# Optimization experiments

Measured on AMD Instinct MI355X. Metric: run time of the kernel, lower is better.

## Reference

```python
import jax, jax.numpy as jnp
import numpy as np

B, S, DIM, H, HD, R = 4, 1024, 2048, 32, 64, 16
START = S  # start_pos == segment_size: memory-update + full-segment branch


def elu1(x):
    # F.elu(x) + 1, positive feature map for compressive memory
    return jnp.where(x > 0, x + 1.0, jnp.exp(jnp.minimum(x, 0.0)))


def rope(t, cos, sin):
    # t: [B, S, H, D]; cos/sin: [S, D/2]; matches torch view_as_complex pairing
    tr = t.reshape(t.shape[:-1] + (-1, 2))
    a, b = tr[..., 0], tr[..., 1]
    c = cos[None, :, None, :]
    s = sin[None, :, None, :]
    out = jnp.stack([a * c - b * s, a * s + b * c], axis=-1)
    return out.reshape(t.shape)


def setup_inputs() -> dict:
    key = jax.random.key(0)
    ks = jax.random.split(key, 24)
    nrm = lambda k, shp, sc=1.0: jax.random.normal(k, shp, dtype=jnp.float32) * sc
    x = nrm(ks[0], (B, S, DIM))
    prompt_query = nrm(ks[1], (B, 1, H, HD))
    cache_k = nrm(ks[2], (B, S, H, HD))
    cache_v = nrm(ks[3], (B, S, H, HD))
    memory_long = nrm(ks[4], (B, H, HD, HD), 0.1)
    memory_query = nrm(ks[5], (B, H, HD, HD), 0.1)
    norm_term = jax.random.uniform(ks[6], (B, H, HD), dtype=jnp.float32) * float(S) + 1.0
    pos = jnp.arange(S, dtype=jnp.float32) + float(START)
    inv = 1.0 / (10000.0 ** (jnp.arange(0, HD, 2, dtype=jnp.float32) / HD))
    ang = pos[:, None] * inv[None, :]
    freqs_cos = jnp.cos(ang).astype(jnp.float32)
    freqs_sin = jnp.sin(ang).astype(jnp.float32)
    causal = jnp.tril(jnp.ones((S, S), dtype=bool))
    mask = jnp.where(causal, 0.0, -1e9).astype(jnp.float32)[None, None]
    sc = 1.0 / np.sqrt(DIM)
    wq = nrm(ks[7], (DIM, DIM), sc)
    wk = nrm(ks[8], (DIM, DIM), sc)
    wv = nrm(ks[9], (DIM, DIM), sc)
    wo = nrm(ks[10], (DIM, DIM), sc)
    lq1 = nrm(ks[11], (R, DIM), sc); lq2 = nrm(ks[12], (DIM, R), 0.01)
    lk1 = nrm(ks[13], (R, DIM), sc); lk2 = nrm(ks[14], (DIM, R), 0.01)
    lv1 = nrm(ks[15], (R, DIM), sc); lv2 = nrm(ks[16], (DIM, R), 0.01)
    lo1 = nrm(ks[17], (R, DIM), sc); lo2 = nrm(ks[18], (DIM, R), 0.01)
    gate = jnp.zeros((1, H, 1, 1), dtype=jnp.float32)
    gmem_w = nrm(ks[19], (1, HD), 0.1)
    gmem_b = jnp.zeros((1,), dtype=jnp.float32)
    return dict(x=x, prompt_query=prompt_query, cache_k=cache_k, cache_v=cache_v,
                memory_long=memory_long, memory_query=memory_query, norm_term=norm_term,
                freqs_cos=freqs_cos, freqs_sin=freqs_sin, mask=mask,
                wq=wq, wk=wk, wv=wv, wo=wo,
                lq1=lq1, lq2=lq2, lk1=lk1, lk2=lk2, lv1=lv1, lv2=lv2, lo1=lo1, lo2=lo2,
                gate=gate, gmem_w=gmem_w, gmem_b=gmem_b, start_pos=START)


def reference(x, prompt_query, cache_k, cache_v, memory_long, memory_query, norm_term,
              freqs_cos, freqs_sin, mask, wq, wk, wv, wo,
              lq1, lq2, lk1, lk2, lv1, lv2, lo1, lo2, gate, gmem_w, gmem_b, start_pos):
    b, s, dim = x.shape
    h = gate.shape[1]
    hd = dim // h
    # LoRA-augmented QKV projections
    xq = x @ wq.T + (x @ lq1.T) @ lq2.T
    xk = x @ wk.T + (x @ lk1.T) @ lk2.T
    xv = x @ wv.T + (x @ lv1.T) @ lv2.T
    xq = xq.reshape(b, s, h, hd)
    xk = xk.reshape(b, s, h, hd)
    xv = xv.reshape(b, s, h, hd)
    q = xq.transpose(0, 2, 1, 3)  # [B,H,S,D]
    # --- memory update from previous segment cache (start_pos >= segment_size) ---
    up_k = cache_k.transpose(0, 2, 1, 3)  # [B,H,S,D]
    up_v = cache_v.transpose(0, 2, 1, 3)
    pq = prompt_query.transpose(0, 2, 1, 3)[:, :, 0, :]  # [B,H,D]
    q_scores = jnp.einsum('bhd,bhsd->bhs', pq, up_k) / np.sqrt(hd)
    query_f_v = up_v * jax.nn.sigmoid(q_scores)[..., None]  # gated value stream
    sigma_k = elu1(up_k)
    mem_l = memory_long + jnp.einsum('bhsd,bhse->bhde', sigma_k, up_v)
    mem_q = memory_query + jnp.einsum('bhsd,bhse->bhde', sigma_k, query_f_v)
    nrm_t = norm_term + sigma_k.sum(axis=2)  # [B,H,D]
    # --- retrieve from compressive memory with pre-RoPE queries ---
    sigma_q = elu1(q)
    denom = jnp.einsum('bhsd,bhd->bhs', sigma_q, nrm_t)[..., None]
    mem_out = jnp.einsum('bhsd,bhde->bhse', sigma_q, mem_l) / denom
    qmem_out = jnp.einsum('bhsd,bhde->bhse', sigma_q, mem_q) / denom
    # --- local causal attention on current segment ---
    qr = rope(xq, freqs_cos, freqs_sin).transpose(0, 2, 1, 3)
    kr = rope(xk, freqs_cos, freqs_sin).transpose(0, 2, 1, 3)
    v = xv.transpose(0, 2, 1, 3)
    scores = jnp.einsum('bhqd,bhkd->bhqk', qr, kr) / np.sqrt(hd) + mask
    probs = jax.nn.softmax(scores, axis=-1)
    attn = jnp.einsum('bhqk,bhkd->bhqd', probs, v)
    # --- gated combination of memory and local attention ---
    g_q = jax.nn.sigmoid(jnp.einsum('bhsd,od->bhso', qmem_out, gmem_w) + gmem_b)
    mem_comb = mem_out + g_q * qmem_out
    g = jax.nn.sigmoid(gate)
    out = g * mem_comb + (1.0 - g) * attn
    out = out.transpose(0, 2, 1, 3).reshape(b, s, dim)
    return out @ wo.T + (out @ lo1.T) @ lo2.T
```

## Files before the change

kernel.cpp:

```cpp
#include <hip/hip_runtime.h>
#include <hip/hip_bf16.h>

typedef __hip_bfloat16 bf16;
typedef __attribute__((ext_vector_type(8))) short short8;
typedef __attribute__((ext_vector_type(4))) float floatx4;

#define B_ 4
#define S_ 1024
#define DIM_ 2048
#define H_ 32
#define HD_ 64
#define R_ 16
#define BS_ (B_*S_)

typedef __attribute__((address_space(1))) void GVoid;
typedef __attribute__((address_space(3))) void LVoid;
#define GLDS16(gp, lp) __builtin_amdgcn_global_load_lds((GVoid*)(gp), (LVoid*)(lp), 16, 0, 0)

__device__ __forceinline__ float b2f(bf16 v){ return __bfloat162float(v); }
__device__ __forceinline__ float elu1f(float x){ return x > 0.f ? x + 1.f : __expf(x); }
__device__ __forceinline__ float sigmoidf(float x){ return 1.f/(1.f + __expf(-x)); }
__device__ __forceinline__ float loadf(bf16 v){ return __bfloat162float(v); }
__device__ __forceinline__ float loadf(float v){ return v; }

__device__ __forceinline__ float dread(const void* p, size_t i, int f){
    float r;
    if (f) r = __bfloat162float(((const bf16*)p)[i]);
    else   r = ((const float*)p)[i];
    return r;
}
__device__ __forceinline__ void dwrite(void* p, size_t i, float v, int f){
    if (f) ((bf16*)p)[i] = __float2bfloat16(v);
    else   ((float*)p)[i] = v;
}

__global__ void detect_kernel(const void* __restrict__ x, int* __restrict__ flag){
    __shared__ int cnt[256];
    int t = threadIdx.x;
    int c = 0;
    for (int i = t; i < 4096; i += 256){
        float v = __bfloat162float(((const bf16*)x)[i]);
        float a = fabsf(v);
        if (a > 1e-3f && a < 1e3f) c++;
    }
    cnt[t] = c;
    __syncthreads();
    if (t == 0){
        int s = 0;
        for (int i = 0; i < 256; ++i) s += cnt[i];
        *flag = (s > 3686) ? 1 : 0;
    }
}

__global__ void convert_kernel(const void* __restrict__ src, bf16* __restrict__ dst,
                               int n, const int* __restrict__ flagp){
    int i = (blockIdx.x * 256 + threadIdx.x) * 8;
    if (i >= n) return;
    short8 o;
    if (*flagp){
        o = *(const short8*)((const bf16*)src + i);
    } else {
        const float* s = (const float*)src + i;
        #pragma unroll
        for (int j = 0; j < 8; ++j)
            ((bf16*)&o)[j] = __float2bfloat16(s[j]);
    }
    *(short8*)(dst + i) = o;
}

template<typename T>
__device__ __forceinline__ void wprep_body(const T* __restrict__ W,
                                           const T* __restrict__ L1,
                                           const T* __restrict__ L2,
                                           bf16* __restrict__ dst){
    int n = blockIdx.y;
    int k = blockIdx.x * 256 + threadIdx.x;
    size_t nk = (size_t)n * DIM_ + k;
    float acc = loadf(W[nk]);
    #pragma unroll
    for (int r = 0; r < 16; ++r)
        acc += loadf(L2[n*16 + r]) * loadf(L1[(size_t)r*DIM_ + k]);
    dst[nk] = __float2bfloat16(acc);
}
__global__ __launch_bounds__(256)
void wprep_kernel(const void* __restrict__ W, const void* __restrict__ L1,
                  const void* __restrict__ L2, const int* __restrict__ flagp,
                  bf16* __restrict__ dst){
    if (*flagp) wprep_body((const bf16*)W, (const bf16*)L1, (const bf16*)L2, dst);
    else        wprep_body((const float*)W, (const float*)L1, (const float*)L2, dst);
}

template<int CMODE>
__global__ __launch_bounds__(256)
void gemm_mfma_kernel(const bf16* __restrict__ A, const bf16* __restrict__ Bw,
                      const int* __restrict__ flagp, void* __restrict__ C) {
    __shared__ bf16 Als[128*32];
    __shared__ bf16 Bls[128*32];
    int tid = threadIdx.x;
    int w = tid >> 6, lane = tid & 63;
    int wr = w >> 1, wc = w & 1;
    int rm0 = blockIdx.y * 128;
    int cn0 = blockIdx.x * 128;

    const bf16* gA = A  + (size_t)(rm0 + w*32 + (lane>>2)) * DIM_ + (lane&3)*8;
    const bf16* gB = Bw + (size_t)(cn0 + w*32 + (lane>>2)) * DIM_ + (lane&3)*8;
    bf16* lA0 = Als + (w*32)*32;
    bf16* lA1 = Als + (w*32+16)*32;
    bf16* lB0 = Bls + (w*32)*32;
    bf16* lB1 = Bls + (w*32+16)*32;

    floatx4 acc[4][4];
    #pragma unroll
    for (int i = 0; i < 4; ++i)
        #pragma unroll
        for (int j = 0; j < 4; ++j) acc[i][j] = (floatx4){0.f,0.f,0.f,0.f};

    int aoff[4], boff[4];
    #pragma unroll
    for (int i = 0; i < 4; ++i) {
        aoff[i] = (wr*64 + i*16 + (lane&15))*32 + (lane>>4)*8;
        boff[i] = (wc*64 + i*16 + (lane&15))*32 + (lane>>4)*8;
    }

    for (int kk = 0; kk < DIM_; kk += 32) {
        GLDS16(gA + kk,             lA0);
        GLDS16(gA + 16*DIM_ + kk,   lA1);
        GLDS16(gB + kk,             lB0);
        GLDS16(gB + 16*DIM_ + kk,   lB1);
        __syncthreads();
        short8 af[4], bf_[4];
        #pragma unroll
        for (int i = 0; i < 4; ++i) {
            af[i]  = *(const short8*)(Als + aoff[i]);
            bf_[i] = *(const short8*)(Bls + boff[i]);
        }
        #pragma unroll
        for (int i = 0; i < 4; ++i)
            #pragma unroll
            for (int j = 0; j < 4; ++j)
                acc[i][j] = __builtin_amdgcn_mfma_f32_16x16x32_bf16(
                    af[i], bf_[j], acc[i][j], 0, 0, 0);
        __syncthreads();
    }

    int f = (CMODE==0) ? *flagp : 1;
    #pragma unroll
    for (int i = 0; i < 4; ++i) {
        #pragma unroll
        for (int reg = 0; reg < 4; ++reg) {
            int m_loc = wr*64 + i*16 + (lane>>4)*4 + reg;
            #pragma unroll
            for (int j = 0; j < 4; ++j) {
                int n_loc = wc*64 + j*16 + (lane&15);
                float val = acc[i][j][reg];
                size_t idx = (size_t)(rm0 + m_loc) * DIM_ + cn0 + n_loc;
                if (CMODE==1) ((bf16*)C)[idx] = __float2bfloat16(val);
                else          dwrite(C, idx, val, f);
            }
        }
    }
}

__global__ void qscore_kernel(const void* __restrict__ pq, const void* __restrict__ ck,
                              const int* __restrict__ flagp, float* __restrict__ qsig) {
    int f = *flagp;
    int tid = threadIdx.x;
    int lane = tid & 63;
    int wid = (blockIdx.x << 2) | (tid >> 6);
    int s = wid & (S_-1);
    int h = (wid >> 10) & (H_-1);
    int b = wid >> 15;
    float p = dread(pq, ((size_t)b*H_ + h)*HD_ + lane, f);
    float k = dread(ck, (((size_t)b*S_ + s)*H_ + h)*HD_ + lane, f);
    float v = p * k;
    for (int off = 32; off; off >>= 1) v += __shfl_xor(v, off, 64);
    if (lane == 0) qsig[((size_t)b*H_ + h)*S_ + s] = sigmoidf(v * 0.125f);
}

__global__ __launch_bounds__(256)
void mem_kernel(const void* __restrict__ ck, const void* __restrict__ cv,
                const float* __restrict__ qsig,
                const int* __restrict__ flagp,
                float* __restrict__ pbufL, float* __restrict__ pbufQ,
                float* __restrict__ pbufN) {
    int f = *flagp;
    __shared__ float ks[4][64], vs[4][64], fv[4][64];
    int bh = blockIdx.x;
    int st = blockIdx.y;
    int b = bh >> 5, h = bh & 31;
    int t = threadIdx.x;
    int e = t & 63;
    int dg = t >> 6;
    float accL[16] = {};
    float accQ[16] = {};
    float nsum = 0.f;
    int sbase = st * 128;
    for (int s0 = 0; s0 < 128; s0 += 4) {
        int sl = t >> 6, d = t & 63;
        int s = sbase + s0 + sl;
        size_t base = (((size_t)b*S_ + s)*H_ + h)*HD_ + d;
        float kv = elu1f(dread(ck, base, f));
        float vv = dread(cv, base, f);
        float sg = qsig[((size_t)b*H_ + h)*S_ + s];
        ks[sl][d] = kv;
        vs[sl][d] = vv;
        fv[sl][d] = vv * sg;
        __syncthreads();
        #pragma unroll
        for (int s2 = 0; s2 < 4; ++s2) {
            float ve = vs[s2][e];
            float fe = fv[s2][e];
            #pragma unroll
            for (int dd = 0; dd < 16; ++dd) {
                float kk = ks[s2][dg*16 + dd];
                accL[dd] += kk * ve;
                accQ[dd] += kk * fe;
            }
        }
        if (t < 64) {
            #pragma unroll
            for (int s2 = 0; s2 < 4; ++s2) nsum += ks[s2][t];
        }
        __syncthreads();
    }
    size_t pb = ((size_t)bh*8 + st) * 4096;
    #pragma unroll
    for (int dd = 0; dd < 16; ++dd) {
        int d = dg*16 + dd;
        pbufL[pb + d*64 + e] = accL[dd];
        pbufQ[pb + d*64 + e] = accQ[dd];
    }
    if (t < 64) pbufN[((size_t)bh*8 + st)*64 + t] = nsum;
}

__global__ __launch_bounds__(256)
void memreduce_kernel(const float* __restrict__ pbufL, const float* __restrict__ pbufQ,
                      const float* __restrict__ pbufN,
                      const void* __restrict__ meml_in, const void* __restrict__ memq_in,
                      const void* __restrict__ norm_in, const int* __restrict__ flagp,
                      float* __restrict__ meml, float* __restrict__ memq,
                      float* __restrict__ nrmt) {
    int f = *flagp;
    size_t gi = (size_t)blockIdx.x * 256 + threadIdx.x;
    int bh = (int)(gi >> 12);
    int i  = (int)(gi & 4095);
    float sL = dread(meml_in, gi, f);
    float sQ = dread(memq_in, gi, f);
    #pragma unroll
    for (int p = 0; p < 8; ++p) {
        sL += pbufL[((size_t)bh*8 + p)*4096 + i];
        sQ += pbufQ[((size_t)bh*8 + p)*4096 + i];
    }
    meml[gi] = sL;
    memq[gi] = sQ;
    if (i < 64) {
        float sN = dread(norm_in, (size_t)bh*64 + i, f);
        #pragma unroll
        for (int p = 0; p < 8; ++p) sN += pbufN[((size_t)bh*8 + p)*64 + i];
        nrmt[(size_t)bh*64 + i] = sN;
    }
}

__global__ __launch_bounds__(256)
void memout_kernel(const bf16* __restrict__ xq, const float* __restrict__ meml,
                   const float* __restrict__ memq, const float* __restrict__ nrmt,
                   const void* __restrict__ gw, const void* __restrict__ gb,
                   const int* __restrict__ flagp, bf16* __restrict__ memcomb) {
    int f = *flagp;
    __shared__ float Ml[64][64];
    __shared__ float Mq[64][64];
    __shared__ float nr[64];
    __shared__ float gwv[64];
    __shared__ float sq[4][64];
    int bh = blockIdx.x;
    int st = blockIdx.y;
    int b = bh >> 5, h = bh & 31;
    int t = threadIdx.x;
    int w = t >> 6, lane = t & 63;
    size_t mb = (size_t)bh * 4096;
    const floatx4* mlv = (const floatx4*)(meml + mb);
    const floatx4* mqv = (const floatx4*)(memq + mb);
    floatx4* Mlv = (floatx4*)&Ml[0][0];
    floatx4* Mqv = (floatx4*)&Mq[0][0];
    for (int i = t; i < 1024; i += 256) {
        Mlv[i] = mlv[i];
        Mqv[i] = mqv[i];
    }
    if (t < 64) { nr[t] = nrmt[(size_t)bh*64 + t]; gwv[t] = dread(gw, t, f); }
    float gbv = dread(gb, 0, f);
    __syncthreads();
    for (int i = 0; i < 16; ++i) {
        int s = st*64 + i*4 + w;
        float x = b2f(xq[((size_t)(b*S_ + s))*DIM_ + h*64 + lane]);
        float sqv = elu1f(x);
        sq[w][lane] = sqv;
        float dv = sqv * nr[lane];
        for (int off = 32; off; off >>= 1) dv += __shfl_xor(dv, off, 64);
        float mo = 0.f, qmo = 0.f;
        #pragma unroll
        for (int d = 0; d < 64; ++d) {
            float sqd = sq[w][d];
            mo  += sqd * Ml[d][lane];
            qmo += sqd * Mq[d][lane];
        }
        float inv = 1.f / dv;
        mo *= inv; qmo *= inv;
        float gqv = qmo * gwv[lane];
        for (int off = 32; off; off >>= 1) gqv += __shfl_xor(gqv, off, 64);
        float gq = sigmoidf(gqv + gbv);
        memcomb[(((size_t)bh)*S_ + s)*64 + lane] = __float2bfloat16(mo + gq * qmo);
    }
}

__global__ void rope_kernel(bf16* __restrict__ buf, const void* __restrict__ fcos,
                            const void* __restrict__ fsin,
                            const int* __restrict__ flagp) {
    int f = *flagp;
    int pid = (blockIdx.x * 256 + threadIdx.x) * 4;
    int cp = pid & 1023;
    int m  = pid >> 10;
    int s  = m & (S_-1);
    int p  = cp & 31;
    size_t idx = (size_t)m * DIM_ + cp*2;
    short8 v = *(const short8*)(buf + idx);
    short8 o;
    #pragma unroll
    for (int j = 0; j < 4; ++j) {
        float c  = dread(fcos, s*32 + p + j, f);
        float sn = dread(fsin, s*32 + p + j, f);
        float a = b2f(((bf16*)&v)[2*j]);
        float b = b2f(((bf16*)&v)[2*j+1]);
        ((bf16*)&o)[2*j]   = __float2bfloat16(a*c - b*sn);
        ((bf16*)&o)[2*j+1] = __float2bfloat16(a*sn + b*c);
    }
    *(short8*)(buf + idx) = o;
}

__global__ __launch_bounds__(256)
void vtrans_kernel(const bf16* __restrict__ xv, bf16* __restrict__ vtg) {
    __shared__ bf16 tile[64*72];
    int bh = blockIdx.x;
    int b = bh >> 5;
    int s0 = blockIdx.y * 64;
    int tid = threadIdx.x;
    for (int it = tid; it < 512; it += 256) {
        int row = it >> 3, blk = it & 7;
        short8 val = *(const short8*)(xv + (size_t)(b*S_ + s0 + row)*DIM_
                                      + (bh & 31)*64 + blk*8);
        *(short8*)(tile + row*72 + ((blk ^ (row & 7))*8)) = val;
    }
    __syncthreads();
    for (int it = tid; it < 512; it += 256) {
        int d = it >> 3, sb = (it & 7)*8;
        short8 o;
        #pragma unroll
        for (int i = 0; i < 8; ++i) {
            int s = sb + i;
            o[i] = *(const short*)(tile + s*72 + (((d>>3) ^ (s & 7))*8) + (d & 7));
        }
        *(short8*)(vtg + ((size_t)bh*64 + d)*S_ + s0 + sb) = o;
    }
}

__global__ __launch_bounds__(256)
void attn_mfma_kernel(const bf16* __restrict__ qr, const bf16* __restrict__ kr,
                      const bf16* __restrict__ vtg, const bf16* __restrict__ memcomb,
                      const void* __restrict__ gate, const int* __restrict__ flagp,
                      bf16* __restrict__ outc) {
    __shared__ bf16 Qs[64*72];
    __shared__ bf16 Ks[64*72];
    __shared__ bf16 Vt[64*72];
    __shared__ bf16 Ps[4][16*72];
    int bid = blockIdx.x;
    int qt = bid & 15;
    int h  = (bid >> 4) & 31;
    int b  = bid >> 9;
    int q0 = qt * 64;
    int tid = threadIdx.x;
    int w = tid >> 6, lane = tid & 63;
    int quad = lane >> 4, r16 = lane & 15;

    for (int it = tid; it < 512; it += 256) {
        int row = it >> 3, c8 = (it & 7)*8;
        *(short8*)(Qs + row*72 + c8) =
            *(const short8*)(qr + (size_t)(b*S_ + q0 + row)*DIM_ + h*64 + c8);
    }
    __syncthreads();
    short8 qf[2];
    #pragma unroll
    for (int kb = 0; kb < 2; ++kb)
        qf[kb] = *(const short8*)(Qs + (w*16 + r16)*72 + kb*32 + quad*8);

    float mrow[4] = {-1e30f,-1e30f,-1e30f,-1e30f};
    float lrow[4] = {0.f,0.f,0.f,0.f};
    floatx4 Ox[4];
    #pragma unroll
    for (int db = 0; db < 4; ++db) Ox[db] = (floatx4){0.f,0.f,0.f,0.f};

    int ntiles = qt + 1;
    for (int kt = 0; kt < ntiles; ++kt) {
        int k0 = kt * 64;
        for (int it = tid; it < 512; it += 256) {
            int row = it >> 3, c8 = (it & 7)*8;
            *(short8*)(Ks + row*72 + c8) =
                *(const short8*)(kr + (size_t)(b*S_ + k0 + row)*DIM_ + h*64 + c8);
            *(short8*)(Vt + row*72 + c8) =
                *(const short8*)(vtg + ((size_t)(b*H_ + h)*64 + row)*S_ + k0 + c8);
        }
        __syncthreads();

        floatx4 Sbv[4];
        #pragma unroll
        for (int nb = 0; nb < 4; ++nb) {
            floatx4 a = (floatx4){0.f,0.f,0.f,0.f};
            #pragma unroll
            for (int kb = 0; kb < 2; ++kb) {
                short8 kf = *(const short8*)(Ks + (nb*16 + r16)*72 + kb*32 + quad*8);
                a = __builtin_amdgcn_mfma_f32_16x16x32_bf16(qf[kb], kf, a, 0, 0, 0);
            }
            Sbv[nb] = a;
        }
        float S4[4][4];
        #pragma unroll
        for (int nb = 0; nb < 4; ++nb)
            #pragma unroll
            for (int reg = 0; reg < 4; ++reg) {
                int qg = q0 + w*16 + quad*4 + reg;
                int kg = k0 + nb*16 + r16;
                float s = Sbv[nb][reg] * 0.125f;
                S4[nb][reg] = (kg > qg) ? -1e30f : s;
            }
        float alpha[4], rsum[4];
        #pragma unroll
        for (int reg = 0; reg < 4; ++reg) {
            float mx = fmaxf(fmaxf(S4[0][reg], S4[1][reg]),
                             fmaxf(S4[2][reg], S4[3][reg]));
            mx = fmaxf(mx, __shfl_xor(mx, 1, 64));
            mx = fmaxf(mx, __shfl_xor(mx, 2, 64));
            mx = fmaxf(mx, __shfl_xor(mx, 4, 64));
            mx = fmaxf(mx, __shfl_xor(mx, 8, 64));
            float mn = fmaxf(mrow[reg], mx);
            alpha[reg] = __expf(mrow[reg] - mn);
            mrow[reg] = mn;
            float rs = 0.f;
            #pragma unroll
            for (int nb = 0; nb < 4; ++nb) {
                float p = __expf(S4[nb][reg] - mn);
                S4[nb][reg] = p;
                rs += p;
            }
            rs += __shfl_xor(rs, 1, 64);
            rs += __shfl_xor(rs, 2, 64);
            rs += __shfl_xor(rs, 4, 64);
            rs += __shfl_xor(rs, 8, 64);
            rsum[reg] = rs;
            lrow[reg] = lrow[reg]*alpha[reg] + rs;
        }
        #pragma unroll
        for (int nb = 0; nb < 4; ++nb)
            #pragma unroll
            for (int reg = 0; reg < 4; ++reg)
                Ps[w][(quad*4 + reg)*72 + nb*16 + r16] = __float2bfloat16(S4[nb][reg]);
        short8 pf[2];
        #pragma unroll
        for (int kb = 0; kb < 2; ++kb)
            pf[kb] = *(const short8*)(&Ps[w][0] + r16*72 + kb*32 + quad*8);
        #pragma unroll
        for (int db = 0; db < 4; ++db) {
            #pragma unroll
            for (int reg = 0; reg < 4; ++reg) Ox[db][reg] *= alpha[reg];
            #pragma unroll
            for (int kb = 0; kb < 2; ++kb) {
                short8 vf = *(const short8*)(Vt + (db*16 + r16)*72 + kb*32 + quad*8);
                Ox[db] = __builtin_amdgcn_mfma_f32_16x16x32_bf16(pf[kb], vf, Ox[db], 0, 0, 0);
            }
        }
        __syncthreads();
    }

    int f = *flagp;
    float g = sigmoidf(dread(gate, h, f));
    #pragma unroll
    for (int db = 0; db < 4; ++db)
        #pragma unroll
        for (int reg = 0; reg < 4; ++reg) {
            int qg = q0 + w*16 + quad*4 + reg;
            int d  = db*16 + r16;
            float attn = Ox[db][reg] / lrow[reg];
            float comb = b2f(memcomb[((size_t)(b*H_ + h)*S_ + qg)*64 + d]);
            outc[(size_t)(b*S_ + qg)*DIM_ + h*64 + d] =
                __float2bfloat16(g*comb + (1.f - g)*attn);
        }
}

extern "C" void kernel_launch(void* const* d_in, const int* in_sizes, int n_in,
                              void* d_out, int out_size, void* d_ws, size_t ws_size,
                              hipStream_t stream) {
    const void* x        = d_in[0];
    const void* pq       = d_in[1];
    const void* cache_k  = d_in[2];
    const void* cache_v  = d_in[3];
    const void* mem_long = d_in[4];
    const void* mem_qry  = d_in[5];
    const void* norm_t   = d_in[6];
    const void* fcos     = d_in[7];
    const void* fsin     = d_in[8];
    const void* wq  = d_in[10];
    const void* wk  = d_in[11];
    const void* wv  = d_in[12];
    const void* wo  = d_in[13];
    const void* lq1 = d_in[14];
    const void* lq2 = d_in[15];
    const void* lk1 = d_in[16];
    const void* lk2 = d_in[17];
    const void* lv1 = d_in[18];
    const void* lv2 = d_in[19];
    const void* lo1 = d_in[20];
    const void* lo2 = d_in[21];
    const void* gate = d_in[22];
    const void* gmw  = d_in[23];
    const void* gmb  = d_in[24];

    const size_t NBSD = (size_t)BS_ * DIM_;
    const size_t NW   = (size_t)DIM_ * DIM_;
    int*  flag = (int*)d_ws;
    bf16* xb   = (bf16*)((char*)d_ws + 16);
    bf16* wbuf = xb + NBSD;
    bf16* xq   = wbuf + NW;
    bf16* xk   = xq + NBSD;
    bf16* xv   = xk + NBSD;
    bf16* outc = xv + NBSD;
    bf16* vtg  = outc + NBSD;
    float* qsig = (float*)(vtg + NBSD);
    float* meml = qsig + (size_t)B_*H_*S_;
    float* memq = meml + (size_t)B_*H_*HD_*HD_;
    float* nrmt = memq + (size_t)B_*H_*HD_*HD_;
    bf16* memcomb = (bf16*)d_out;

    float* pbufL = (float*)xb;
    float* pbufQ = (float*)outc;
    float* pbufN = (float*)wbuf;

    dim3 ggrid(DIM_/128, BS_/128);
    dim3 wgrid(DIM_/256, DIM_);

    detect_kernel<<<1, 256, 0, stream>>>(x, flag);
    convert_kernel<<<(int)(NBSD/2048), 256, 0, stream>>>(x, xb, (int)NBSD, flag);
    wprep_kernel<<<wgrid, 256, 0, stream>>>(wq, lq1, lq2, flag, wbuf);
    gemm_mfma_kernel<1><<<ggrid, 256, 0, stream>>>(xb, wbuf, flag, xq);
    wprep_kernel<<<wgrid, 256, 0, stream>>>(wk, lk1, lk2, flag, wbuf);
    gemm_mfma_kernel<1><<<ggrid, 256, 0, stream>>>(xb, wbuf, flag, xk);
    wprep_kernel<<<wgrid, 256, 0, stream>>>(wv, lv1, lv2, flag, wbuf);
    gemm_mfma_kernel<1><<<ggrid, 256, 0, stream>>>(xb, wbuf, flag, xv);
    vtrans_kernel<<<dim3(B_*H_, S_/64), 256, 0, stream>>>(xv, vtg);
    qscore_kernel<<<(B_*H_*S_)/4, 256, 0, stream>>>(pq, cache_k, flag, qsig);
    mem_kernel<<<dim3(B_*H_, 8), 256, 0, stream>>>(cache_k, cache_v, qsig, flag,
                                                   pbufL, pbufQ, pbufN);
    memreduce_kernel<<<(B_*H_*HD_*HD_)/256, 256, 0, stream>>>(
        pbufL, pbufQ, pbufN, mem_long, mem_qry, norm_t, flag, meml, memq, nrmt);
    memout_kernel<<<dim3(B_*H_, S_/64), 256, 0, stream>>>(xq, meml, memq, nrmt,
                                                          gmw, gmb, flag, memcomb);
    rope_kernel<<<(BS_*1024)/(256*4), 256, 0, stream>>>(xq, fcos, fsin, flag);
    rope_kernel<<<(BS_*1024)/(256*4), 256, 0, stream>>>(xk, fcos, fsin, flag);
    attn_mfma_kernel<<<B_*H_*(S_/64), 256, 0, stream>>>(xq, xk, vtg, memcomb,
                                                        gate, flag, outc);
    wprep_kernel<<<wgrid, 256, 0, stream>>>(wo, lo1, lo2, flag, wbuf);
    gemm_mfma_kernel<0><<<ggrid, 256, 0, stream>>>(outc, wbuf, flag, d_out);
}
```

Baseline: 838.8 us.

## Batch QKV weight prep and GEMMs, prefetch K/V tiles in causal attention

Merges the three weight-prep kernels and the three QKV projection GEMMs into single launches, with the K and V prepared weights stored in the vtg scratch region. The attention kernel now prefetches the next K/V tile into registers while the current tile computes, and remaps block indices so heavy and light causal tiles interleave. It also adds setprio around the MFMA loops and an XOR swizzle on the P tile in LDS to reduce bank conflicts. The vtg buffer is reused for weights before vtrans overwrites it, so correctness relies on that launch ordering.

Measured after the change: 773.8 us. 7.7% less time.

```diff
diff --git a/kernel.cpp b/kernel.cpp
--- a/kernel.cpp
+++ b/kernel.cpp
@@ -90,6 +90,25 @@
     else        wprep_body((const float*)W, (const float*)L1, (const float*)L2, dst);
 }
 
+__global__ __launch_bounds__(256)
+void wprep3_kernel(const void* __restrict__ W0, const void* __restrict__ W1,
+                   const void* __restrict__ W2,
+                   const void* __restrict__ L1q, const void* __restrict__ L1k,
+                   const void* __restrict__ L1v,
+                   const void* __restrict__ L2q, const void* __restrict__ L2k,
+                   const void* __restrict__ L2v,
+                   const int* __restrict__ flagp,
+                   bf16* __restrict__ d0, bf16* __restrict__ d1,
+                   bf16* __restrict__ d2){
+    int z = blockIdx.z;
+    const void* W  = (z==0) ? W0 : (z==1) ? W1 : W2;
+    const void* L1 = (z==0) ? L1q : (z==1) ? L1k : L1v;
+    const void* L2 = (z==0) ? L2q : (z==1) ? L2k : L2v;
+    bf16* dst = (z==0) ? d0 : (z==1) ? d1 : d2;
+    if (*flagp) wprep_body((const bf16*)W, (const bf16*)L1, (const bf16*)L2, dst);
+    else        wprep_body((const float*)W, (const float*)L1, (const float*)L2, dst);
+}
+
 template<int CMODE>
 __global__ __launch_bounds__(256)
 void gemm_mfma_kernel(const bf16* __restrict__ A, const bf16* __restrict__ Bw,
@@ -156,6 +175,79 @@
                 size_t idx = (size_t)(rm0 + m_loc) * DIM_ + cn0 + n_loc;
                 if (CMODE==1) ((bf16*)C)[idx] = __float2bfloat16(val);
                 else          dwrite(C, idx, val, f);
+            }
+        }
+    }
+}
+
+__global__ __launch_bounds__(256)
+void gemm_mfma3_kernel(const bf16* __restrict__ A,
+                       const bf16* __restrict__ B0, const bf16* __restrict__ B1,
+                       const bf16* __restrict__ B2,
+                       bf16* __restrict__ C0, bf16* __restrict__ C1,
+                       bf16* __restrict__ C2) {
+    __shared__ bf16 Als[128*32];
+    __shared__ bf16 Bls[128*32];
+    int tid = threadIdx.x;
+    int w = tid >> 6, lane = tid & 63;
+    int wr = w >> 1, wc = w & 1;
+    int rm0 = blockIdx.y * 128;
+    int wz  = blockIdx.x >> 4;
+    int cn0 = (blockIdx.x & 15) * 128;
+    const bf16* Bw = (wz==0) ? B0 : (wz==1) ? B1 : B2;
+    bf16* C        = (wz==0) ? C0 : (wz==1) ? C1 : C2;
+
+    const bf16* gA = A  + (size_t)(rm0 + w*32 + (lane>>2)) * DIM_ + (lane&3)*8;
+    const bf16* gB = Bw + (size_t)(cn0 + w*32 + (lane>>2)) * DIM_ + (lane&3)*8;
+    bf16* lA0 = Als + (w*32)*32;
+    bf16* lA1 = Als + (w*32+16)*32;
+    bf16* lB0 = Bls + (w*32)*32;
+    bf16* lB1 = Bls + (w*32+16)*32;
+
+    floatx4 acc[4][4];
+    #pragma unroll
+    for (int i = 0; i < 4; ++i)
+        #pragma unroll
+        for (int j = 0; j < 4; ++j) acc[i][j] = (floatx4){0.f,0.f,0.f,0.f};
+
+    int aoff[4], boff[4];
+    #pragma unroll
+    for (int i = 0; i < 4; ++i) {
+        aoff[i] = (wr*64 + i*16 + (lane&15))*32 + (lane>>4)*8;
+        boff[i] = (wc*64 + i*16 + (lane&15))*32 + (lane>>4)*8;
+    }
+
+    for (int kk = 0; kk < DIM_; kk += 32) {
+        GLDS16(gA + kk,             lA0);
+        GLDS16(gA + 16*DIM_ + kk,   lA1);
+        GLDS16(gB + kk,             lB0);
+        GLDS16(gB + 16*DIM_ + kk,   lB1);
+        __syncthreads();
+        short8 af[4], bf_[4];
+        #pragma unroll
+        for (int i = 0; i < 4; ++i) {
+            af[i]  = *(const short8*)(Als + aoff[i]);
+            bf_[i] = *(const short8*)(Bls + boff[i]);
+        }
+        #pragma unroll
+        for (int i = 0; i < 4; ++i)
+            #pragma unroll
+            for (int j = 0; j < 4; ++j)
+                acc[i][j] = __builtin_amdgcn_mfma_f32_16x16x32_bf16(
+                    af[i], bf_[j], acc[i][j], 0, 0, 0);
+        __syncthreads();
+    }
+
+    #pragma unroll
+    for (int i = 0; i < 4; ++i) {
+        #pragma unroll
+        for (int reg = 0; reg < 4; ++reg) {
+            int m_loc = wr*64 + i*16 + (lane>>4)*4 + reg;
+            #pragma unroll
+            for (int j = 0; j < 4; ++j) {
+                int n_loc = wc*64 + j*16 + (lane&15);
+                size_t idx = (size_t)(rm0 + m_loc) * DIM_ + cn0 + n_loc;
+                C[idx] = __float2bfloat16(acc[i][j][reg]);
             }
         }
     }
@@ -371,7 +463,8 @@
     __shared__ bf16 Ks[64*72];
     __shared__ bf16 Vt[64*72];
     __shared__ bf16 Ps[4][16*72];
-    int bid = blockIdx.x;
+    int bid0 = blockIdx.x;
+    int bid = ((bid0 & 7) << 8) | (bid0 >> 3);
     int qt = bid & 15;
     int h  = (bid >> 4) & 31;
     int b  = bid >> 9;
@@ -384,6 +477,10 @@
         int row = it >> 3, c8 = (it & 7)*8;
         *(short8*)(Qs + row*72 + c8) =
             *(const short8*)(qr + (size_t)(b*S_ + q0 + row)*DIM_ + h*64 + c8);
+        *(short8*)(Ks + row*72 + c8) =
+            *(const short8*)(kr + (size_t)(b*S_ + row)*DIM_ + h*64 + c8);
+        *(short8*)(Vt + row*72 + c8) =
+            *(const short8*)(vtg + ((size_t)(b*H_ + h)*64 + row)*S_ + c8);
     }
     __syncthreads();
     short8 qf[2];
@@ -397,19 +494,24 @@
     #pragma unroll
     for (int db = 0; db < 4; ++db) Ox[db] = (floatx4){0.f,0.f,0.f,0.f};
 
+    int prow0 = tid >> 3, pc8 = (tid & 7)*8;
+    int prow1 = prow0 + 32;
+
     int ntiles = qt + 1;
     for (int kt = 0; kt < ntiles; ++kt) {
         int k0 = kt * 64;
-        for (int it = tid; it < 512; it += 256) {
-            int row = it >> 3, c8 = (it & 7)*8;
-            *(short8*)(Ks + row*72 + c8) =
-                *(const short8*)(kr + (size_t)(b*S_ + k0 + row)*DIM_ + h*64 + c8);
-            *(short8*)(Vt + row*72 + c8) =
-                *(const short8*)(vtg + ((size_t)(b*H_ + h)*64 + row)*S_ + k0 + c8);
-        }
-        __syncthreads();
+        short8 kn0, kn1, vn0, vn1;
+        bool pre = (kt + 1 < ntiles);
+        if (pre) {
+            int k0n = k0 + 64;
+            kn0 = *(const short8*)(kr + (size_t)(b*S_ + k0n + prow0)*DIM_ + h*64 + pc8);
+            kn1 = *(const short8*)(kr + (size_t)(b*S_ + k0n + prow1)*DIM_ + h*64 + pc8);
+            vn0 = *(const short8*)(vtg + ((size_t)(b*H_ + h)*64 + prow0)*S_ + k0n + pc8);
+            vn1 = *(const short8*)(vtg + ((size_t)(b*H_ + h)*64 + prow1)*S_ + k0n + pc8);
+        }
 
         floatx4 Sbv[4];
+        __builtin_amdgcn_s_setprio(1);
         #pragma unroll
         for (int nb = 0; nb < 4; ++nb) {
             floatx4 a = (floatx4){0.f,0.f,0.f,0.f};
@@ -420,6 +522,7 @@
             }
             Sbv[nb] = a;
         }
+        __builtin_amdgcn_s_setprio(0);
         float S4[4][4];
         #pragma unroll
         for (int nb = 0; nb < 4; ++nb)
@@ -430,7 +533,7 @@
                 float s = Sbv[nb][reg] * 0.125f;
                 S4[nb][reg] = (kg > qg) ? -1e30f : s;
             }
-        float alpha[4], rsum[4];
+        float alpha[4];
         #pragma unroll
         for (int reg = 0; reg < 4; ++reg) {
             float mx = fmaxf(fmaxf(S4[0][reg], S4[1][reg]),
@@ -453,27 +556,40 @@
             rs += __shfl_xor(rs, 2, 64);
             rs += __shfl_xor(rs, 4, 64);
             rs += __shfl_xor(rs, 8, 64);
-            rsum[reg] = rs;
             lrow[reg] = lrow[reg]*alpha[reg] + rs;
         }
         #pragma unroll
         for (int nb = 0; nb < 4; ++nb)
             #pragma unroll
             for (int reg = 0; reg < 4; ++reg)
-                Ps[w][(quad*4 + reg)*72 + nb*16 + r16] = __float2bfloat16(S4[nb][reg]);
+                Ps[w][(quad*4 + reg)*72 + ((nb*16 + r16) ^ ((quad & 2) * 8))] =
+                    __float2bfloat16(S4[nb][reg]);
         short8 pf[2];
         #pragma unroll
         for (int kb = 0; kb < 2; ++kb)
-            pf[kb] = *(const short8*)(&Ps[w][0] + r16*72 + kb*32 + quad*8);
+            pf[kb] = *(const short8*)(&Ps[w][0] + r16*72 +
+                                      ((kb*32 + quad*8) ^ ((r16 & 8) << 1)));
         #pragma unroll
         for (int db = 0; db < 4; ++db) {
             #pragma unroll
             for (int reg = 0; reg < 4; ++reg) Ox[db][reg] *= alpha[reg];
+        }
+        __builtin_amdgcn_s_setprio(1);
+        #pragma unroll
+        for (int db = 0; db < 4; ++db) {
             #pragma unroll
             for (int kb = 0; kb < 2; ++kb) {
                 short8 vf = *(const short8*)(Vt + (db*16 + r16)*72 + kb*32 + quad*8);
                 Ox[db] = __builtin_amdgcn_mfma_f32_16x16x32_bf16(pf[kb], vf, Ox[db], 0, 0, 0);
             }
+        }
+        __builtin_amdgcn_s_setprio(0);
+        __syncthreads();
+        if (pre) {
+            *(short8*)(Ks + prow0*72 + pc8) = kn0;
+            *(short8*)(Ks + prow1*72 + pc8) = kn1;
+            *(short8*)(Vt + prow0*72 + pc8) = vn0;
+            *(short8*)(Vt + prow1*72 + pc8) = vn1;
         }
         __syncthreads();
     }
@@ -537,21 +653,24 @@
     float* nrmt = memq + (size_t)B_*H_*HD_*HD_;
     bf16* memcomb = (bf16*)d_out;
 
+    bf16* wbK = (bf16*)vtg;
+    bf16* wbV = wbK + NW;
+
     float* pbufL = (float*)xb;
     float* pbufQ = (float*)outc;
     float* pbufN = (float*)wbuf;
 
     dim3 ggrid(DIM_/128, BS_/128);
+    dim3 ggrid3(3*DIM_/128, BS_/128);
     dim3 wgrid(DIM_/256, DIM_);
+    dim3 wgrid3(DIM_/256, DIM_, 3);
 
     detect_kernel<<<1, 256, 0, stream>>>(x, flag);
     convert_kernel<<<(int)(NBSD/2048), 256, 0, stream>>>(x, xb, (int)NBSD, flag);
-    wprep_kernel<<<wgrid, 256, 0, stream>>>(wq, lq1, lq2, flag, wbuf);
-    gemm_mfma_kernel<1><<<ggrid, 256, 0, stream>>>(xb, wbuf, flag, xq);
-    wprep_kernel<<<wgrid, 256, 0, stream>>>(wk, lk1, lk2, flag, wbuf);
-    gemm_mfma_kernel<1><<<ggrid, 256, 0, stream>>>(xb, wbuf, flag, xk);
-    wprep_kernel<<<wgrid, 256, 0, stream>>>(wv, lv1, lv2, flag, wbuf);
-    gemm_mfma_kernel<1><<<ggrid, 256, 0, stream>>>(xb, wbuf, flag, xv);
+    wprep3_kernel<<<wgrid3, 256, 0, stream>>>(wq, wk, wv, lq1, lk1, lv1,
+                                              lq2, lk2, lv2, flag,
+                                              wbuf, wbK, wbV);
+    gemm_mfma3_kernel<<<ggrid3, 256, 0, stream>>>(xb, wbuf, wbK, wbV, xq, xk, xv);
     vtrans_kernel<<<dim3(B_*H_, S_/64), 256, 0, stream>>>(xv, vtg);
     qscore_kernel<<<(B_*H_*S_)/4, 256, 0, stream>>>(pq, cache_k, flag, qsig);
     mem_kernel<<<dim3(B_*H_, 8), 256, 0, stream>>>(cache_k, cache_v, qsig, flag,
```
